# Performance work log

Hardware: AMD Instinct MI355X
Metric: run time of the kernel (lower is better)

Reference implementation:

```python
import jax, jax.numpy as jnp
import numpy as np

N_NODES = 100000
N_EDGES = 1600000
D = 128
LEAKY_SLOPE = 0.01  # torch nn.LeakyReLU default


def setup_inputs() -> dict:
    key = jax.random.key(0)
    k1, k2, k3, k4 = jax.random.split(key, 4)
    in_states = jax.random.normal(k1, (N_NODES, D), dtype=jnp.float32)
    edges = jax.random.randint(k2, (2, N_EDGES), 0, N_NODES, dtype=jnp.int64)
    # Linear weights, kaiming-uniform-ish scale
    W_msg = jax.random.normal(k3, (D, D), dtype=jnp.float32) / np.sqrt(D)
    attn_w = jax.random.normal(k4, (2 * D,), dtype=jnp.float32) / np.sqrt(2 * D)
    W_res = jnp.eye(D, dtype=jnp.float32)  # eye-initialized, frozen residual proj
    passthrough_coef = jnp.ones((1,), dtype=jnp.float32)
    return {"in_states": in_states, "edges": edges, "W_msg": W_msg,
            "attn_w": attn_w, "W_res": W_res, "passthrough_coef": passthrough_coef}


def reference(in_states, edges, W_msg, attn_w, W_res, passthrough_coef):
    n_nodes = in_states.shape[0]
    src, dst = edges[0], edges[1]

    # message transform (dropout in eval mode -> identity)
    messages = in_states @ W_msg.T                       # [N, D]

    # attention score: Linear(2D->1) on cat([m_from, m_to]) == split dot products
    s_from = messages @ attn_w[:D]                       # [N]
    s_to = messages @ attn_w[D:]                         # [N]
    e = s_from[src] + s_to[dst]                          # [E]
    e = jnp.where(e >= 0, e, LEAKY_SLOPE * e)            # LeakyReLU

    # indexed (segment) softmax over destination nodes
    seg_max = jax.ops.segment_max(e, dst, num_segments=n_nodes)
    e_exp = jnp.exp(e - seg_max[dst])
    seg_sum = jax.ops.segment_sum(e_exp, dst, num_segments=n_nodes)
    alpha = e_exp / seg_sum[dst]                         # [E]

    # weighted scatter-add aggregation
    scaled = alpha[:, None] * messages[src]              # [E, D]
    merged = jax.ops.segment_sum(scaled, dst, num_segments=n_nodes)  # [N, D]

    new_states_res = jax.nn.relu(merged)
    old_passthrough = (in_states @ W_res.T) * jax.nn.sigmoid(passthrough_coef[0])
    return old_passthrough + new_states_res
```

## Files before the change

kernel.cpp:

```cpp
#include <hip/hip_runtime.h>
#include <hip/hip_fp16.h>


#define DD 128
#define NPB 32
#define LEAKY 0.01f

#define FMA4(A, XS, W)                                        \
  A.x = fmaf((XS), (W).x, A.x); A.y = fmaf((XS), (W).y, A.y); \
  A.z = fmaf((XS), (W).z, A.z); A.w = fmaf((XS), (W).w, A.w)

__global__ void k_transpose2(const float* __restrict__ Wm, const float* __restrict__ Wr,
                             float* __restrict__ WTm, float* __restrict__ WTr) {
  int idx = blockIdx.x * blockDim.x + threadIdx.x;
  if (idx < DD * DD) {
    int j = idx >> 7, k = idx & (DD - 1);
    WTm[k * DD + j] = Wm[idx];
    WTr[k * DD + j] = Wr[idx];
  }
}

__global__ void k_zero(int* __restrict__ p, int n) {
  int i = blockIdx.x * blockDim.x + threadIdx.x;
  if (i < n) p[i] = 0;
}

__global__ void k_detect(const int* __restrict__ e, int* __restrict__ flag) {
  if (threadIdx.x == 0 && blockIdx.x == 0) {
    int all0 = 1;
    for (int i = 0; i < 64; ++i)
      if (e[2 * i + 1] != 0) { all0 = 0; break; }
    flag[0] = all0;
  }
}

__global__ void k_eye(const float* __restrict__ Wr, int* __restrict__ eyeflag) {
  __shared__ int ok_s;
  if (threadIdx.x == 0) ok_s = 1;
  __syncthreads();
  int ok = 1;
  for (int i = threadIdx.x; i < DD * DD; i += 256) {
    float expect = ((i >> 7) == (i & (DD - 1))) ? 1.f : 0.f;
    if (Wr[i] != expect) ok = 0;
  }
  if (!ok) ok_s = 0;
  __syncthreads();
  if (threadIdx.x == 0) eyeflag[0] = ok_s;
}

__global__ __launch_bounds__(256) void k_msg(
    const float* __restrict__ x, const float* __restrict__ WTm,
    const float* __restrict__ WTr, const float* __restrict__ attn_w,
    const float* __restrict__ coef, const int* __restrict__ eyeflag, int n_nodes,
    __half* __restrict__ mh, float* __restrict__ s_from,
    float* __restrict__ s_to, float* __restrict__ out) {
  __shared__ float4 lw4[32 * 32];
  __shared__ float4 lx4[NPB * 32];
  __shared__ float lds_aw[2 * DD];
  const int t = threadIdx.x;
  const int base = blockIdx.x * NPB;
  const int nvalid = min(NPB, n_nodes - base);

  const float4* xs = (const float4*)(x + (size_t)base * DD);
  const int nflt4 = nvalid * 32;
  for (int i = t; i < nflt4; i += 256) lx4[i] = xs[i];
  if (t < 2 * DD) lds_aw[t] = attn_w[t];

  const int j4 = t & 31;
  const int g = t >> 5;
  const int r0 = (g * 4 + 0) * 32, r1 = r0 + 32, r2 = r1 + 32, r3 = r2 + 32;

  float4 a0, a1, a2, a3;

#define GEMM128(WT)                                                           \
  a0 = a1 = a2 = a3 = make_float4(0.f, 0.f, 0.f, 0.f);                        \
  _Pragma("unroll 1")                                                         \
  for (int chunk = 0; chunk < 4; ++chunk) {                                   \
    __syncthreads();                                                          \
    const float4* wsrc = (const float4*)((WT) + chunk * 32 * DD);             \
    lw4[t] = wsrc[t];                                                         \
    lw4[t + 256] = wsrc[t + 256];                                             \
    lw4[t + 512] = wsrc[t + 512];                                             \
    lw4[t + 768] = wsrc[t + 768];                                             \
    __syncthreads();                                                          \
    const int xb = chunk * 8;                                                 \
    _Pragma("unroll 2")                                                       \
    for (int k = 0; k < 32; k += 4) {                                         \
      float4 w0 = lw4[(k + 0) * 32 + j4];                                     \
      float4 w1 = lw4[(k + 1) * 32 + j4];                                     \
      float4 w2 = lw4[(k + 2) * 32 + j4];                                     \
      float4 w3 = lw4[(k + 3) * 32 + j4];                                     \
      float4 x0 = lx4[r0 + xb + (k >> 2)];                                    \
      float4 x1 = lx4[r1 + xb + (k >> 2)];                                    \
      float4 x2 = lx4[r2 + xb + (k >> 2)];                                    \
      float4 x3 = lx4[r3 + xb + (k >> 2)];                                    \
      FMA4(a0, x0.x, w0); FMA4(a0, x0.y, w1);                                 \
      FMA4(a0, x0.z, w2); FMA4(a0, x0.w, w3);                                 \
      FMA4(a1, x1.x, w0); FMA4(a1, x1.y, w1);                                 \
      FMA4(a1, x1.z, w2); FMA4(a1, x1.w, w3);                                 \
      FMA4(a2, x2.x, w0); FMA4(a2, x2.y, w1);                                 \
      FMA4(a2, x2.z, w2); FMA4(a2, x2.w, w3);                                 \
      FMA4(a3, x3.x, w0); FMA4(a3, x3.y, w1);                                 \
      FMA4(a3, x3.z, w2); FMA4(a3, x3.w, w3);                                 \
    }                                                                         \
  }

  GEMM128(WTm);
  {
    float4 av[4] = {a0, a1, a2, a3};
#pragma unroll
    for (int b = 0; b < 4; ++b) {
      int n = g * 4 + b;
      if (n < nvalid) {
        int gn = base + n;
        float4 v = av[b];
        union { __half2 h2[2]; uint2 u; } pk;
        pk.h2[0] = __floats2half2_rn(v.x, v.y);
        pk.h2[1] = __floats2half2_rn(v.z, v.w);
        ((uint2*)(mh + (size_t)gn * DD))[j4] = pk.u;
        float sf = v.x * lds_aw[4 * j4] + v.y * lds_aw[4 * j4 + 1] +
                   v.z * lds_aw[4 * j4 + 2] + v.w * lds_aw[4 * j4 + 3];
        float stv = v.x * lds_aw[DD + 4 * j4] + v.y * lds_aw[DD + 4 * j4 + 1] +
                    v.z * lds_aw[DD + 4 * j4 + 2] + v.w * lds_aw[DD + 4 * j4 + 3];
#pragma unroll
        for (int m = 16; m; m >>= 1) {
          sf += __shfl_xor(sf, m, 32);
          stv += __shfl_xor(stv, m, 32);
        }
        if (j4 == 0) { s_from[gn] = sf; s_to[gn] = stv; }
      }
    }
  }

  const float sig = 1.f / (1.f + __expf(-coef[0]));
  if (eyeflag[0]) {
    float4* od = (float4*)(out + (size_t)base * DD);
    for (int i = t; i < nflt4; i += 256) {
      float4 v = lx4[i];
      v.x *= sig; v.y *= sig; v.z *= sig; v.w *= sig;
      od[i] = v;
    }
  } else {
    GEMM128(WTr);
    float4 av[4] = {a0, a1, a2, a3};
#pragma unroll
    for (int b = 0; b < 4; ++b) {
      int n = g * 4 + b;
      if (n < nvalid) {
        int gn = base + n;
        float4 v = av[b];
        v.x *= sig; v.y *= sig; v.z *= sig; v.w *= sig;
        ((float4*)(out + (size_t)gn * DD))[j4] = v;
      }
    }
  }
#undef GEMM128
}

__global__ void k_count(const int* __restrict__ edges, int n_edges, int n_nodes,
                        const int* __restrict__ flag, int* __restrict__ deg) {
  int i = blockIdx.x * blockDim.x + threadIdx.x;
  if (i < n_edges) {
    int is64 = flag[0];
    int d = is64 ? edges[2 * n_edges + 2 * i] : edges[n_edges + i];
    if ((unsigned)d < (unsigned)n_nodes) atomicAdd(&deg[d], 1);
  }
}

__global__ __launch_bounds__(256) void k_scan_a(const int* __restrict__ deg, int n,
                                                int* __restrict__ outp,
                                                int* __restrict__ bsum) {
  __shared__ int lds[256];
  const int t = threadIdx.x;
  const int base = blockIdx.x * 1024 + t * 4;
  int v0 = 0, v1 = 0, v2 = 0, v3 = 0;
  if (base + 3 < n) {
    int4 q = *(const int4*)(deg + base);
    v0 = q.x; v1 = q.y; v2 = q.z; v3 = q.w;
  } else {
    if (base + 0 < n) v0 = deg[base + 0];
    if (base + 1 < n) v1 = deg[base + 1];
    if (base + 2 < n) v2 = deg[base + 2];
    if (base + 3 < n) v3 = deg[base + 3];
  }
  const int tsum = v0 + v1 + v2 + v3;
  int val = tsum;
  lds[t] = val;
  __syncthreads();
  for (int off = 1; off < 256; off <<= 1) {
    int a = (t >= off) ? lds[t - off] : 0;
    __syncthreads();
    val += a;
    lds[t] = val;
    __syncthreads();
  }
  int o0 = val - tsum;
  int o1 = o0 + v0, o2 = o1 + v1, o3 = o2 + v2;
  if (base + 0 < n) outp[base + 0] = o0;
  if (base + 1 < n) outp[base + 1] = o1;
  if (base + 2 < n) outp[base + 2] = o2;
  if (base + 3 < n) outp[base + 3] = o3;
  if (t == 255) bsum[blockIdx.x] = val;
}

__global__ void k_scan_b(int* __restrict__ bsum, int nb) {
  __shared__ int lds[256];
  const int t = threadIdx.x;
  int v = (t < nb) ? bsum[t] : 0;
  int val = v;
  lds[t] = val;
  __syncthreads();
  for (int off = 1; off < 256; off <<= 1) {
    int a = (t >= off) ? lds[t - off] : 0;
    __syncthreads();
    val += a;
    lds[t] = val;
    __syncthreads();
  }
  if (t < nb) bsum[t] = val - v;
}

__global__ void k_scan_c(int* __restrict__ row_start, int* __restrict__ cursor,
                         const int* __restrict__ bsum, int n, int n_edges) {
  const int t = threadIdx.x;
  const int off = bsum[blockIdx.x];
  const int base = blockIdx.x * 1024 + t * 4;
#pragma unroll
  for (int c = 0; c < 4; ++c) {
    int idx = base + c;
    if (idx < n) {
      int r = row_start[idx] + off;
      row_start[idx] = r;
      cursor[idx] = r;
    }
  }
  if (blockIdx.x == 0 && t == 0) row_start[n] = n_edges;
}

__global__ void k_scatter(const int* __restrict__ edges, int n_edges, int n_nodes,
                          const int* __restrict__ flag, int* __restrict__ cursor,
                          int* __restrict__ srcs) {
  int i = blockIdx.x * blockDim.x + threadIdx.x;
  if (i < n_edges) {
    int is64 = flag[0];
    int d = is64 ? edges[2 * n_edges + 2 * i] : edges[n_edges + i];
    int s = is64 ? edges[2 * i] : edges[i];
    if ((unsigned)d < (unsigned)n_nodes) {
      int pos = atomicAdd(&cursor[d], 1);
      srcs[pos] = s;
    }
  }
}

__global__ __launch_bounds__(256) void k_agg(
    const int* __restrict__ row_start, const int* __restrict__ srcs,
    const float* __restrict__ s_from, const float* __restrict__ s_to,
    const __half* __restrict__ mh, int n_nodes, float* __restrict__ out) {
  const int lane = threadIdx.x & 63;
  const int v = blockIdx.x * 4 + (threadIdx.x >> 6);
  if (v >= n_nodes) return;
  const int start = row_start[v];
  const int end = row_start[v + 1];
  if (start >= end) return;
  const float st = s_to[v];

  float wsum = 0.f;
  float ax = 0.f, ay = 0.f;
  for (int cbase = start; cbase < end; cbase += 64) {
    const int cnt = min(64, end - cbase);
    int s = 0;
    float w = 0.f;
    if (lane < cnt) {
      s = srcs[cbase + lane];
      if ((unsigned)s >= (unsigned)n_nodes) s = 0;
      float xx = s_from[s] + st;
      xx = (xx >= 0.f) ? xx : LEAKY * xx;
      w = __expf(xx);
    }
    wsum += w;
#pragma unroll 4
    for (int i = 0; i < cnt; ++i) {
      int si = __shfl(s, i, 64);
      float wi = __shfl(w, i, 64);
      const __half2 m2h = ((const __half2*)(mh + (size_t)si * DD))[lane];
      const float2 mf = __half22float2(m2h);
      ax = fmaf(wi, mf.x, ax);
      ay = fmaf(wi, mf.y, ay);
    }
  }
#pragma unroll
  for (int m = 32; m; m >>= 1) wsum += __shfl_xor(wsum, m, 64);
  const float inv = 1.f / wsum;
  ax *= inv; ay *= inv;
  ax = (ax > 0.f) ? ax : 0.f;
  ay = (ay > 0.f) ? ay : 0.f;
  float2* orow = (float2*)(out + (size_t)v * DD);
  float2 po = orow[lane];
  orow[lane] = make_float2(po.x + ax, po.y + ay);
}

extern "C" void kernel_launch(void* const* d_in, const int* in_sizes, int n_in,
                              void* d_out, int out_size, void* d_ws, size_t ws_size,
                              hipStream_t stream) {
  const float* x = (const float*)d_in[0];
  const int* edges = (const int*)d_in[1];
  const float* Wm = (const float*)d_in[2];
  const float* aw = (const float*)d_in[3];
  const float* Wr = (const float*)d_in[4];
  const float* coef = (const float*)d_in[5];
  float* out = (float*)d_out;

  const int N = in_sizes[0] / DD;
  const int E = in_sizes[1] / 2;

  const size_t need = ((size_t)N * DD * 2 + 256)
                    + 2 * ((size_t)N * 4 + 256)
                    + 2 * ((size_t)DD * DD * 4 + 256)
                    + 3 * ((size_t)N * 4 + 512)
                    + 2048
                    + (size_t)E * 4 + 256;
  if (ws_size < need) return;

  char* w = (char*)d_ws;
  auto alloc = [&](size_t bytes) {
    char* p = w;
    w += (bytes + 255) & ~(size_t)255;
    return p;
  };
  __half* mh     = (__half*)alloc((size_t)N * DD * 2);
  float* s_from  = (float*)alloc((size_t)N * 4);
  float* s_to    = (float*)alloc((size_t)N * 4);
  float* WTm     = (float*)alloc((size_t)DD * DD * 4);
  float* WTr     = (float*)alloc((size_t)DD * DD * 4);
  int*   deg     = (int*)alloc((size_t)N * 4);
  int*   row_start = (int*)alloc((size_t)(N + 1) * 4);
  int*   cursor  = (int*)alloc((size_t)N * 4);
  int*   bsum    = (int*)alloc(256 * 4);
  int*   flag    = (int*)alloc(256);
  int*   srcs    = (int*)alloc((size_t)E * 4);

  k_detect<<<1, 64, 0, stream>>>(edges, flag);
  k_eye<<<1, 256, 0, stream>>>(Wr, flag + 1);
  k_transpose2<<<(DD * DD + 255) / 256, 256, 0, stream>>>(Wm, Wr, WTm, WTr);
  k_zero<<<(N + 255) / 256, 256, 0, stream>>>(deg, N);
  k_msg<<<(N + NPB - 1) / NPB, 256, 0, stream>>>(x, WTm, WTr, aw, coef, flag + 1,
                                                 N, mh, s_from, s_to, out);
  k_count<<<(E + 255) / 256, 256, 0, stream>>>(edges, E, N, flag, deg);
  const int nb1 = (N + 1023) / 1024;
  k_scan_a<<<nb1, 256, 0, stream>>>(deg, N, row_start, bsum);
  k_scan_b<<<1, 256, 0, stream>>>(bsum, nb1);
  k_scan_c<<<nb1, 256, 0, stream>>>(row_start, cursor, bsum, N, E);
  k_scatter<<<(E + 255) / 256, 256, 0, stream>>>(edges, E, N, flag, cursor, srcs);
  k_agg<<<(N + 3) / 4, 256, 0, stream>>>(row_start, srcs, s_from, s_to,
                                         mh, N, out);
}
```

Measured before the change: 486.6 us.

## Bucket destinations into 16-node groups with shared-memory atomic aggregation

Replaces the per-node CSR build (count, three-pass scan, scatter) with per-bucket counting over groups of 16 destination nodes, a single-block scan, and a scatter of packed (src, local dst) entries. Aggregation now runs one block per bucket: it computes attention weights into LDS, then accumulates weighted fp16 message rows into an LDS accumulator via shared atomics. This cuts scan kernels and launches, but adds contention on global bucket atomics and many LDS float atomics per edge.

```diff
diff --git a/kernel.cpp b/kernel.cpp
--- a/kernel.cpp
+++ b/kernel.cpp
@@ -5,6 +5,9 @@
 #define DD 128
 #define NPB 32
 #define LEAKY 0.01f
+#define BSH 4
+#define BSZ 16
+#define CHK 1024
 
 #define FMA4(A, XS, W)                                        \
   A.x = fmaf((XS), (W).x, A.x); A.y = fmaf((XS), (W).y, A.y); \
@@ -157,146 +160,136 @@
 #undef GEMM128
 }
 
-__global__ void k_count(const int* __restrict__ edges, int n_edges, int n_nodes,
-                        const int* __restrict__ flag, int* __restrict__ deg) {
+__global__ void k_bcount(const int* __restrict__ edges, int n_edges, int n_nodes,
+                         const int* __restrict__ flag, int* __restrict__ bcnt) {
   int i = blockIdx.x * blockDim.x + threadIdx.x;
   if (i < n_edges) {
-    int is64 = flag[0];
-    int d = is64 ? edges[2 * n_edges + 2 * i] : edges[n_edges + i];
-    if ((unsigned)d < (unsigned)n_nodes) atomicAdd(&deg[d], 1);
-  }
-}
-
-__global__ __launch_bounds__(256) void k_scan_a(const int* __restrict__ deg, int n,
-                                                int* __restrict__ outp,
-                                                int* __restrict__ bsum) {
+    int d = flag[0] ? ((const int2*)edges)[n_edges + i].x : edges[n_edges + i];
+    if ((unsigned)d < (unsigned)n_nodes) atomicAdd(&bcnt[d >> BSH], 1);
+  }
+}
+
+__global__ __launch_bounds__(256) void k_bscan(const int* __restrict__ cnt, int nb,
+                                               int* __restrict__ bstart,
+                                               int* __restrict__ bcursor) {
   __shared__ int lds[256];
+  __shared__ int carry_s;
   const int t = threadIdx.x;
-  const int base = blockIdx.x * 1024 + t * 4;
-  int v0 = 0, v1 = 0, v2 = 0, v3 = 0;
-  if (base + 3 < n) {
-    int4 q = *(const int4*)(deg + base);
-    v0 = q.x; v1 = q.y; v2 = q.z; v3 = q.w;
-  } else {
-    if (base + 0 < n) v0 = deg[base + 0];
-    if (base + 1 < n) v1 = deg[base + 1];
-    if (base + 2 < n) v2 = deg[base + 2];
-    if (base + 3 < n) v3 = deg[base + 3];
-  }
-  const int tsum = v0 + v1 + v2 + v3;
-  int val = tsum;
-  lds[t] = val;
+  if (t == 0) carry_s = 0;
   __syncthreads();
-  for (int off = 1; off < 256; off <<= 1) {
-    int a = (t >= off) ? lds[t - off] : 0;
-    __syncthreads();
-    val += a;
+  const int nchunks = (nb + 1023) / 1024;
+  for (int c = 0; c < nchunks; ++c) {
+    const int carry = carry_s;
+    const int base = c * 1024 + t * 4;
+    int v0 = 0, v1 = 0, v2 = 0, v3 = 0;
+    if (base + 0 < nb) v0 = cnt[base + 0];
+    if (base + 1 < nb) v1 = cnt[base + 1];
+    if (base + 2 < nb) v2 = cnt[base + 2];
+    if (base + 3 < nb) v3 = cnt[base + 3];
+    const int tsum = v0 + v1 + v2 + v3;
+    int val = tsum;
     lds[t] = val;
     __syncthreads();
-  }
-  int o0 = val - tsum;
-  int o1 = o0 + v0, o2 = o1 + v1, o3 = o2 + v2;
-  if (base + 0 < n) outp[base + 0] = o0;
-  if (base + 1 < n) outp[base + 1] = o1;
-  if (base + 2 < n) outp[base + 2] = o2;
-  if (base + 3 < n) outp[base + 3] = o3;
-  if (t == 255) bsum[blockIdx.x] = val;
-}
-
-__global__ void k_scan_b(int* __restrict__ bsum, int nb) {
-  __shared__ int lds[256];
-  const int t = threadIdx.x;
-  int v = (t < nb) ? bsum[t] : 0;
-  int val = v;
-  lds[t] = val;
-  __syncthreads();
-  for (int off = 1; off < 256; off <<= 1) {
-    int a = (t >= off) ? lds[t - off] : 0;
-    __syncthreads();
-    val += a;
-    lds[t] = val;
-    __syncthreads();
-  }
-  if (t < nb) bsum[t] = val - v;
-}
-
-__global__ void k_scan_c(int* __restrict__ row_start, int* __restrict__ cursor,
-                         const int* __restrict__ bsum, int n, int n_edges) {
-  const int t = threadIdx.x;
-  const int off = bsum[blockIdx.x];
-  const int base = blockIdx.x * 1024 + t * 4;
-#pragma unroll
-  for (int c = 0; c < 4; ++c) {
-    int idx = base + c;
-    if (idx < n) {
-      int r = row_start[idx] + off;
-      row_start[idx] = r;
-      cursor[idx] = r;
-    }
-  }
-  if (blockIdx.x == 0 && t == 0) row_start[n] = n_edges;
-}
-
-__global__ void k_scatter(const int* __restrict__ edges, int n_edges, int n_nodes,
-                          const int* __restrict__ flag, int* __restrict__ cursor,
-                          int* __restrict__ srcs) {
+    for (int off = 1; off < 256; off <<= 1) {
+      int a = (t >= off) ? lds[t - off] : 0;
+      __syncthreads();
+      val += a;
+      lds[t] = val;
+      __syncthreads();
+    }
+    int o0 = carry + val - tsum;
+    int o1 = o0 + v0, o2 = o1 + v1, o3 = o2 + v2;
+    if (base + 0 < nb) { bstart[base + 0] = o0; bcursor[base + 0] = o0; }
+    if (base + 1 < nb) { bstart[base + 1] = o1; bcursor[base + 1] = o1; }
+    if (base + 2 < nb) { bstart[base + 2] = o2; bcursor[base + 2] = o2; }
+    if (base + 3 < nb) { bstart[base + 3] = o3; bcursor[base + 3] = o3; }
+    __syncthreads();
+    if (t == 255) carry_s = carry + val;
+    __syncthreads();
+  }
+  if (t == 0) bstart[nb] = carry_s;
+}
+
+__global__ void k_bscatter(const int* __restrict__ edges, int n_edges, int n_nodes,
+                           const int* __restrict__ flag, int* __restrict__ bcursor,
+                           int* __restrict__ packed) {
   int i = blockIdx.x * blockDim.x + threadIdx.x;
   if (i < n_edges) {
-    int is64 = flag[0];
-    int d = is64 ? edges[2 * n_edges + 2 * i] : edges[n_edges + i];
-    int s = is64 ? edges[2 * i] : edges[i];
+    int d, s;
+    if (flag[0]) {
+      d = ((const int2*)edges)[n_edges + i].x;
+      s = ((const int2*)edges)[i].x;
+    } else {
+      d = edges[n_edges + i];
+      s = edges[i];
+    }
     if ((unsigned)d < (unsigned)n_nodes) {
-      int pos = atomicAdd(&cursor[d], 1);
-      srcs[pos] = s;
-    }
-  }
-}
-
-__global__ __launch_bounds__(256) void k_agg(
-    const int* __restrict__ row_start, const int* __restrict__ srcs,
+      if ((unsigned)s >= (unsigned)n_nodes) s = 0;
+      int pos = atomicAdd(&bcursor[d >> BSH], 1);
+      packed[pos] = (s << BSH) | (d & (BSZ - 1));
+    }
+  }
+}
+
+__global__ __launch_bounds__(256) void k_bagg(
+    const int* __restrict__ bstart, const int* __restrict__ packed,
     const float* __restrict__ s_from, const float* __restrict__ s_to,
     const __half* __restrict__ mh, int n_nodes, float* __restrict__ out) {
-  const int lane = threadIdx.x & 63;
-  const int v = blockIdx.x * 4 + (threadIdx.x >> 6);
-  if (v >= n_nodes) return;
-  const int start = row_start[v];
-  const int end = row_start[v + 1];
-  if (start >= end) return;
-  const float st = s_to[v];
-
-  float wsum = 0.f;
-  float ax = 0.f, ay = 0.f;
-  for (int cbase = start; cbase < end; cbase += 64) {
-    const int cnt = min(64, end - cbase);
-    int s = 0;
-    float w = 0.f;
-    if (lane < cnt) {
-      s = srcs[cbase + lane];
-      if ((unsigned)s >= (unsigned)n_nodes) s = 0;
-      float xx = s_from[s] + st;
-      xx = (xx >= 0.f) ? xx : LEAKY * xx;
-      w = __expf(xx);
-    }
-    wsum += w;
-#pragma unroll 4
-    for (int i = 0; i < cnt; ++i) {
-      int si = __shfl(s, i, 64);
-      float wi = __shfl(w, i, 64);
-      const __half2 m2h = ((const __half2*)(mh + (size_t)si * DD))[lane];
-      const float2 mf = __half22float2(m2h);
-      ax = fmaf(wi, mf.x, ax);
-      ay = fmaf(wi, mf.y, ay);
-    }
-  }
-#pragma unroll
-  for (int m = 32; m; m >>= 1) wsum += __shfl_xor(wsum, m, 64);
-  const float inv = 1.f / wsum;
-  ax *= inv; ay *= inv;
-  ax = (ax > 0.f) ? ax : 0.f;
-  ay = (ay > 0.f) ? ay : 0.f;
-  float2* orow = (float2*)(out + (size_t)v * DD);
-  float2 po = orow[lane];
-  orow[lane] = make_float2(po.x + ax, po.y + ay);
+  __shared__ float acc[BSZ][DD];
+  __shared__ float wbuf[CHK];
+  __shared__ int   ibuf[CHK];
+  __shared__ float wsum[BSZ];
+  __shared__ float stl[BSZ];
+  const int t = threadIdx.x;
+  const int b = blockIdx.x;
+  const int nbase = b << BSH;
+  for (int i = t; i < BSZ * DD; i += 256) ((float*)acc)[i] = 0.f;
+  if (t < BSZ) {
+    wsum[t] = 0.f;
+    int node = nbase + t;
+    stl[t] = (node < n_nodes) ? s_to[node] : 0.f;
+  }
+  const int start = bstart[b], end = bstart[b + 1];
+  __syncthreads();
+  const int wave = t >> 6, lane = t & 63;
+  for (int cb = start; cb < end; cb += CHK) {
+    const int cn = min(CHK, end - cb);
+    for (int i = t; i < cn; i += 256) {
+      int u = packed[cb + i];
+      int s = u >> BSH, dl = u & (BSZ - 1);
+      float e = s_from[s] + stl[dl];
+      e = (e >= 0.f) ? e : LEAKY * e;
+      float w = __expf(e);
+      wbuf[i] = w;
+      ibuf[i] = u;
+      atomicAdd(&wsum[dl], w);
+    }
+    __syncthreads();
+    for (int i = wave; i < cn; i += 4) {
+      int u = ibuf[i];
+      float w = wbuf[i];
+      int s = u >> BSH, dl = u & (BSZ - 1);
+      float2 mf = __half22float2(((const __half2*)(mh + (size_t)s * DD))[lane]);
+      atomicAdd(&acc[dl][2 * lane], w * mf.x);
+      atomicAdd(&acc[dl][2 * lane + 1], w * mf.y);
+    }
+    __syncthreads();
+  }
+  for (int dl = wave; dl < BSZ; dl += 4) {
+    int node = nbase + dl;
+    if (node >= n_nodes) break;
+    float ws = wsum[dl];
+    if (ws > 0.f) {
+      float inv = 1.f / ws;
+      float ax = acc[dl][2 * lane] * inv;
+      float ay = acc[dl][2 * lane + 1] * inv;
+      ax = ax > 0.f ? ax : 0.f;
+      ay = ay > 0.f ? ay : 0.f;
+      float2* orow = (float2*)(out + (size_t)node * DD);
+      float2 po = orow[lane];
+      orow[lane] = make_float2(po.x + ax, po.y + ay);
+    }
+  }
 }
 
 extern "C" void kernel_launch(void* const* d_in, const int* in_sizes, int n_in,
@@ -312,12 +305,13 @@
 
   const int N = in_sizes[0] / DD;
   const int E = in_sizes[1] / 2;
+  const int nb = (N + BSZ - 1) / BSZ;
 
   const size_t need = ((size_t)N * DD * 2 + 256)
                     + 2 * ((size_t)N * 4 + 256)
                     + 2 * ((size_t)DD * DD * 4 + 256)
-                    + 3 * ((size_t)N * 4 + 512)
-                    + 2048
+                    + 3 * ((size_t)(nb + 1) * 4 + 512)
+                    + 1024
                     + (size_t)E * 4 + 256;
   if (ws_size < need) return;
 
@@ -332,25 +326,20 @@
   float* s_to    = (float*)alloc((size_t)N * 4);
   float* WTm     = (float*)alloc((size_t)DD * DD * 4);
   float* WTr     = (float*)alloc((size_t)DD * DD * 4);
-  int*   deg     = (int*)alloc((size_t)N * 4);
-  int*   row_start = (int*)alloc((size_t)(N + 1) * 4);
-  int*   cursor  = (int*)alloc((size_t)N * 4);
-  int*   bsum    = (int*)alloc(256 * 4);
+  int*   bcnt    = (int*)alloc((size_t)nb * 4);
+  int*   bstart  = (int*)alloc((size_t)(nb + 1) * 4);
+  int*   bcursor = (int*)alloc((size_t)nb * 4);
   int*   flag    = (int*)alloc(256);
-  int*   srcs    = (int*)alloc((size_t)E * 4);
+  int*   packed  = (int*)alloc((size_t)E * 4);
 
   k_detect<<<1, 64, 0, stream>>>(edges, flag);
   k_eye<<<1, 256, 0, stream>>>(Wr, flag + 1);
   k_transpose2<<<(DD * DD + 255) / 256, 256, 0, stream>>>(Wm, Wr, WTm, WTr);
-  k_zero<<<(N + 255) / 256, 256, 0, stream>>>(deg, N);
+  k_zero<<<(nb + 255) / 256, 256, 0, stream>>>(bcnt, nb);
   k_msg<<<(N + NPB - 1) / NPB, 256, 0, stream>>>(x, WTm, WTr, aw, coef, flag + 1,
                                                  N, mh, s_from, s_to, out);
-  k_count<<<(E + 255) / 256, 256, 0, stream>>>(edges, E, N, flag, deg);
-  const int nb1 = (N + 1023) / 1024;
-  k_scan_a<<<nb1, 256, 0, stream>>>(deg, N, row_start, bsum);
-  k_scan_b<<<1, 256, 0, stream>>>(bsum, nb1);
-  k_scan_c<<<nb1, 256, 0, stream>>>(row_start, cursor, bsum, N, E);
-  k_scatter<<<(E + 255) / 256, 256, 0, stream>>>(edges, E, N, flag, cursor, srcs);
-  k_agg<<<(N + 3) / 4, 256, 0, stream>>>(row_start, srcs, s_from, s_to,
-                                         mh, N, out);
-}
+  k_bcount<<<(E + 255) / 256, 256, 0, stream>>>(edges, E, N, flag, bcnt);
+  k_bscan<<<1, 256, 0, stream>>>(bcnt, nb, bstart, bcursor);
+  k_bscatter<<<(E + 255) / 256, 256, 0, stream>>>(edges, E, N, flag, bcursor, packed);
+  k_bagg<<<nb, 256, 0, stream>>>(bstart, packed, s_from, s_to, mh, N, out);
+}
```

After: 1.407 ms. +189.1%, slower.
